# Kernel optimization log

Measured on AMD Instinct MI355X. Metric: run time of the kernel, lower is better.

Reference implementation:

```python
import jax, jax.numpy as jnp
import numpy as np

N_POINTS = 1_000_000
FDIM = 32
GRID = 128  # gx = gy = gz = ceil(20 / 0.15625) = 128
LO, HI = -10.0, 10.0
INIT_STD = 0.05


def setup_inputs() -> dict:
    key = jax.random.key(0)
    k1, k2 = jax.random.split(key)
    # query points inside the bound
    x = jax.random.uniform(k1, (N_POINTS, 3), jnp.float32, LO, HI)
    # dense voxel feature grid, layout [C, D, H, W] (squeezed batch dim)
    feature = jax.random.normal(k2, (FDIM, GRID, GRID, GRID), jnp.float32) * INIT_STD
    return {"x": x, "feature": feature}


def reference(x, feature):
    # normalize_coordinates: map bound -> [-1, 1] per axis (x, y, z order)
    coords = 2.0 * (x - LO) / (HI - LO) - 1.0  # [N, 3]

    C, D, H, W = feature.shape
    # grid_sample, align_corners=False: pixel = ((c + 1) * size - 1) / 2
    fx = ((coords[:, 0] + 1.0) * W - 1.0) * 0.5
    fy = ((coords[:, 1] + 1.0) * H - 1.0) * 0.5
    fz = ((coords[:, 2] + 1.0) * D - 1.0) * 0.5

    x0f, y0f, z0f = jnp.floor(fx), jnp.floor(fy), jnp.floor(fz)
    wx, wy, wz = fx - x0f, fy - y0f, fz - z0f  # trilinear fractions
    x0 = x0f.astype(jnp.int32)
    y0 = y0f.astype(jnp.int32)
    z0 = z0f.astype(jnp.int32)

    feat_flat = feature.reshape(C, -1)  # [C, D*H*W]
    out = jnp.zeros((C, x.shape[0]), dtype=feature.dtype)
    for dz in (0, 1):
        for dy in (0, 1):
            for dx in (0, 1):
                xi, yi, zi = x0 + dx, y0 + dy, z0 + dz
                w = ((wx if dx else 1.0 - wx)
                     * (wy if dy else 1.0 - wy)
                     * (wz if dz else 1.0 - wz))
                # padding_mode='zeros': out-of-range corners contribute 0
                valid = ((xi >= 0) & (xi < W) & (yi >= 0) & (yi < H)
                         & (zi >= 0) & (zi < D))
                idx = ((jnp.clip(zi, 0, D - 1) * H + jnp.clip(yi, 0, H - 1)) * W
                       + jnp.clip(xi, 0, W - 1))
                vals = feat_flat[:, idx]  # gather -> [C, N]
                out = out + vals * (w * valid).astype(feature.dtype)[None, :]
    # transpose(0, 1) -> [N, fdim]
    return out.T
```

## Files before the change

### kernel.cpp

```cpp
#include <hip/hip_runtime.h>
#include <hip/hip_fp16.h>


constexpr int   GD      = 128;
constexpr long long SPATIAL = (long long)GD * GD * GD;
constexpr int   FD      = 32;
constexpr float PLO     = -10.0f;
constexpr float PHI     = 10.0f;

typedef float nfloat4 __attribute__((ext_vector_type(4)));

__global__ __launch_bounds__(256) void transpose_feat_h(
    const float* __restrict__ f, __half* __restrict__ o) {
    __shared__ float lds[64][FD + 1];
    const int t  = threadIdx.x;
    const long long s0 = (long long)blockIdx.x * 64;
    const int sl = t & 63;
    const int cq = t >> 6;
#pragma unroll
    for (int it = 0; it < 8; ++it) {
        const int c = it * 4 + cq;
        lds[sl][c] =
            __builtin_nontemporal_load(f + (size_t)c * SPATIAL + s0 + sl);
    }
    __syncthreads();
    const int c0 = (t & 15) * 2;
    const int sw = t >> 4;
#pragma unroll
    for (int it = 0; it < 4; ++it) {
        const int s = sw + it * 16;
        __half2 h;
        h.x = __float2half(lds[s][c0]);
        h.y = __float2half(lds[s][c0 + 1]);
        *reinterpret_cast<__half2*>(o + (size_t)(s0 + s) * FD + c0) = h;
    }
}

__global__ __launch_bounds__(256) void trilerp_h(
    const float* __restrict__ x, const __half* __restrict__ ft,
    float* __restrict__ out, int npts) {
    const int tid = blockIdx.x * 256 + threadIdx.x;
    const int n = tid >> 2;
    if (n >= npts) return;
    const int j = tid & 3;

    const float px = x[3 * n + 0];
    const float py = x[3 * n + 1];
    const float pz = x[3 * n + 2];

    const float cx = 2.0f * (px - PLO) / (PHI - PLO) - 1.0f;
    const float cy = 2.0f * (py - PLO) / (PHI - PLO) - 1.0f;
    const float cz = 2.0f * (pz - PLO) / (PHI - PLO) - 1.0f;
    const float fx = ((cx + 1.0f) * GD - 1.0f) * 0.5f;
    const float fy = ((cy + 1.0f) * GD - 1.0f) * 0.5f;
    const float fz = ((cz + 1.0f) * GD - 1.0f) * 0.5f;

    const float x0f = floorf(fx), y0f = floorf(fy), z0f = floorf(fz);
    const float wx = fx - x0f, wy = fy - y0f, wz = fz - z0f;
    const int x0 = (int)x0f, y0 = (int)y0f, z0 = (int)z0f;

    float acc[8] = {0.f, 0.f, 0.f, 0.f, 0.f, 0.f, 0.f, 0.f};
#pragma unroll
    for (int dz = 0; dz < 2; ++dz) {
#pragma unroll
        for (int dy = 0; dy < 2; ++dy) {
#pragma unroll
            for (int dx = 0; dx < 2; ++dx) {
                const int xi = x0 + dx, yi = y0 + dy, zi = z0 + dz;
                const bool valid = ((unsigned)xi < (unsigned)GD) &
                                   ((unsigned)yi < (unsigned)GD) &
                                   ((unsigned)zi < (unsigned)GD);
                float w = (dx ? wx : 1.0f - wx) * (dy ? wy : 1.0f - wy) *
                          (dz ? wz : 1.0f - wz);
                w = valid ? w : 0.0f;
                const int xc = min(max(xi, 0), GD - 1);
                const int yc = min(max(yi, 0), GD - 1);
                const int zc = min(max(zi, 0), GD - 1);
                const size_t idx = (size_t)(zc * GD + yc) * GD + xc;
                const nfloat4 raw = *reinterpret_cast<const nfloat4*>(
                    ft + idx * FD + j * 8);
                const __half2* h2 = reinterpret_cast<const __half2*>(&raw);
#pragma unroll
                for (int k = 0; k < 4; ++k) {
                    const float2 fv = __half22float2(h2[k]);
                    acc[2 * k + 0] = fmaf(fv.x, w, acc[2 * k + 0]);
                    acc[2 * k + 1] = fmaf(fv.y, w, acc[2 * k + 1]);
                }
            }
        }
    }
    float* op = out + (size_t)n * FD + j * 8;
    nfloat4 o0 = {acc[0], acc[1], acc[2], acc[3]};
    nfloat4 o1 = {acc[4], acc[5], acc[6], acc[7]};
    __builtin_nontemporal_store(o0, reinterpret_cast<nfloat4*>(op));
    __builtin_nontemporal_store(o1, reinterpret_cast<nfloat4*>(op) + 1);
}

__global__ __launch_bounds__(256) void trilerp_direct(
    const float* __restrict__ x, const float* __restrict__ f,
    float* __restrict__ out, int npts) {
    const int tid = blockIdx.x * 256 + threadIdx.x;
    const int n = tid >> 3;
    if (n >= npts) return;
    const int j = tid & 7;

    const float px = x[3 * n + 0];
    const float py = x[3 * n + 1];
    const float pz = x[3 * n + 2];
    const float cx = 2.0f * (px - PLO) / (PHI - PLO) - 1.0f;
    const float cy = 2.0f * (py - PLO) / (PHI - PLO) - 1.0f;
    const float cz = 2.0f * (pz - PLO) / (PHI - PLO) - 1.0f;
    const float fx = ((cx + 1.0f) * GD - 1.0f) * 0.5f;
    const float fy = ((cy + 1.0f) * GD - 1.0f) * 0.5f;
    const float fz = ((cz + 1.0f) * GD - 1.0f) * 0.5f;
    const float x0f = floorf(fx), y0f = floorf(fy), z0f = floorf(fz);
    const float wx = fx - x0f, wy = fy - y0f, wz = fz - z0f;
    const int x0 = (int)x0f, y0 = (int)y0f, z0 = (int)z0f;

    float acc[4] = {0.f, 0.f, 0.f, 0.f};
#pragma unroll
    for (int dz = 0; dz < 2; ++dz)
#pragma unroll
        for (int dy = 0; dy < 2; ++dy)
#pragma unroll
            for (int dx = 0; dx < 2; ++dx) {
                const int xi = x0 + dx, yi = y0 + dy, zi = z0 + dz;
                const bool valid = ((unsigned)xi < (unsigned)GD) &
                                   ((unsigned)yi < (unsigned)GD) &
                                   ((unsigned)zi < (unsigned)GD);
                float w = (dx ? wx : 1.0f - wx) * (dy ? wy : 1.0f - wy) *
                          (dz ? wz : 1.0f - wz);
                w = valid ? w : 0.0f;
                const int xc = min(max(xi, 0), GD - 1);
                const int yc = min(max(yi, 0), GD - 1);
                const int zc = min(max(zi, 0), GD - 1);
                const size_t idx = (size_t)(zc * GD + yc) * GD + xc;
#pragma unroll
                for (int k = 0; k < 4; ++k)
                    acc[k] = fmaf(f[(size_t)(j * 4 + k) * SPATIAL + idx], w, acc[k]);
            }
#pragma unroll
    for (int k = 0; k < 4; ++k) out[(size_t)n * FD + j * 4 + k] = acc[k];
}

extern "C" void kernel_launch(void* const* d_in, const int* in_sizes, int n_in,
                              void* d_out, int out_size, void* d_ws, size_t ws_size,
                              hipStream_t stream) {
    const float* x    = (const float*)d_in[0];
    const float* feat = (const float*)d_in[1];
    float*       out  = (float*)d_out;
    const int npts = in_sizes[0] / 3;

    const size_t need = (size_t)SPATIAL * FD * sizeof(__half);

    if (ws_size >= need) {
        __half* fth = (__half*)d_ws;
        transpose_feat_h<<<(int)(SPATIAL / 64), 256, 0, stream>>>(feat, fth);
        const int gblocks = (npts * 4 + 255) / 256;
        trilerp_h<<<gblocks, 256, 0, stream>>>(x, fth, out, npts);
    } else {
        const int gblocks = (npts * 8 + 255) / 256;
        trilerp_direct<<<gblocks, 256, 0, stream>>>(x, feat, out, npts);
    }
}
```

Baseline: 497.7 us.

## Bin query points by z-slab before trilinear gather to improve locality

```diff
diff --git a/kernel.cpp b/kernel.cpp
--- a/kernel.cpp
+++ b/kernel.cpp
@@ -7,8 +7,16 @@
 constexpr int   FD      = 32;
 constexpr float PLO     = -10.0f;
 constexpr float PHI     = 10.0f;
+constexpr int   NBUCKET = 129;
 
 typedef float nfloat4 __attribute__((ext_vector_type(4)));
+
+__device__ __forceinline__ int z_bucket(float pz) {
+    const float cz = 2.0f * (pz - PLO) / (PHI - PLO) - 1.0f;
+    const float fz = ((cz + 1.0f) * GD - 1.0f) * 0.5f;
+    int zb = (int)floorf(fz) + 1;
+    return min(max(zb, 0), NBUCKET - 1);
+}
 
 __global__ __launch_bounds__(256) void transpose_feat_h(
     const float* __restrict__ f, __half* __restrict__ o) {
@@ -36,17 +44,57 @@
     }
 }
 
-__global__ __launch_bounds__(256) void trilerp_h(
-    const float* __restrict__ x, const __half* __restrict__ ft,
-    float* __restrict__ out, int npts) {
-    const int tid = blockIdx.x * 256 + threadIdx.x;
-    const int n = tid >> 2;
+__global__ __launch_bounds__(256) void hist_kernel(
+    const float* __restrict__ x, int* __restrict__ hist, int npts) {
+    __shared__ int h[NBUCKET];
+    const int t = threadIdx.x;
+    if (t < NBUCKET) h[t] = 0;
+    __syncthreads();
+    const int n = blockIdx.x * 256 + t;
+    if (n < npts) {
+        const int zb = z_bucket(x[3 * n + 2]);
+        atomicAdd(&h[zb], 1);
+    }
+    __syncthreads();
+    if (t < NBUCKET && h[t]) atomicAdd(&hist[t], h[t]);
+}
+
+__global__ void scan_hist(const int* __restrict__ hist,
+                          int* __restrict__ cursor) {
+    if (threadIdx.x == 0 && blockIdx.x == 0) {
+        int run = 0;
+        for (int b = 0; b < NBUCKET; ++b) {
+            cursor[b] = run;
+            run += hist[b];
+        }
+    }
+}
+
+__global__ __launch_bounds__(256) void scatter_kernel(
+    const float* __restrict__ x, int* __restrict__ cursor,
+    nfloat4* __restrict__ binned, int npts) {
+    const int n = blockIdx.x * 256 + threadIdx.x;
     if (n >= npts) return;
-    const int j = tid & 3;
-
     const float px = x[3 * n + 0];
     const float py = x[3 * n + 1];
     const float pz = x[3 * n + 2];
+    const int zb = z_bucket(pz);
+    const int pos = atomicAdd(&cursor[zb], 1);
+    nfloat4 rec = {px, py, pz, __int_as_float(n)};
+    binned[pos] = rec;
+}
+
+__global__ __launch_bounds__(256) void trilerp_b(
+    const nfloat4* __restrict__ binned, const __half* __restrict__ ft,
+    float* __restrict__ out, int npts) {
+    const int tid = blockIdx.x * 256 + threadIdx.x;
+    const int i = tid >> 2;
+    if (i >= npts) return;
+    const int j = tid & 3;
+
+    const nfloat4 rec = binned[i];
+    const float px = rec.x, py = rec.y, pz = rec.z;
+    const int n = __float_as_int(rec.w);
 
     const float cx = 2.0f * (px - PLO) / (PHI - PLO) - 1.0f;
     const float cy = 2.0f * (py - PLO) / (PHI - PLO) - 1.0f;
@@ -96,13 +144,13 @@
     __builtin_nontemporal_store(o1, reinterpret_cast<nfloat4*>(op) + 1);
 }
 
-__global__ __launch_bounds__(256) void trilerp_direct(
-    const float* __restrict__ x, const float* __restrict__ f,
+__global__ __launch_bounds__(256) void trilerp_h(
+    const float* __restrict__ x, const __half* __restrict__ ft,
     float* __restrict__ out, int npts) {
     const int tid = blockIdx.x * 256 + threadIdx.x;
-    const int n = tid >> 3;
+    const int n = tid >> 2;
     if (n >= npts) return;
-    const int j = tid & 7;
+    const int j = tid & 3;
 
     const float px = x[3 * n + 0];
     const float py = x[3 * n + 1];
@@ -117,7 +165,7 @@
     const float wx = fx - x0f, wy = fy - y0f, wz = fz - z0f;
     const int x0 = (int)x0f, y0 = (int)y0f, z0 = (int)z0f;
 
-    float acc[4] = {0.f, 0.f, 0.f, 0.f};
+    float acc[8] = {0.f, 0.f, 0.f, 0.f, 0.f, 0.f, 0.f, 0.f};
 #pragma unroll
     for (int dz = 0; dz < 2; ++dz)
 #pragma unroll
@@ -135,6 +183,62 @@
                 const int yc = min(max(yi, 0), GD - 1);
                 const int zc = min(max(zi, 0), GD - 1);
                 const size_t idx = (size_t)(zc * GD + yc) * GD + xc;
+                const nfloat4 raw = *reinterpret_cast<const nfloat4*>(
+                    ft + idx * FD + j * 8);
+                const __half2* h2 = reinterpret_cast<const __half2*>(&raw);
+#pragma unroll
+                for (int k = 0; k < 4; ++k) {
+                    const float2 fv = __half22float2(h2[k]);
+                    acc[2 * k + 0] = fmaf(fv.x, w, acc[2 * k + 0]);
+                    acc[2 * k + 1] = fmaf(fv.y, w, acc[2 * k + 1]);
+                }
+            }
+    float* op = out + (size_t)n * FD + j * 8;
+    nfloat4 o0 = {acc[0], acc[1], acc[2], acc[3]};
+    nfloat4 o1 = {acc[4], acc[5], acc[6], acc[7]};
+    __builtin_nontemporal_store(o0, reinterpret_cast<nfloat4*>(op));
+    __builtin_nontemporal_store(o1, reinterpret_cast<nfloat4*>(op) + 1);
+}
+
+__global__ __launch_bounds__(256) void trilerp_direct(
+    const float* __restrict__ x, const float* __restrict__ f,
+    float* __restrict__ out, int npts) {
+    const int tid = blockIdx.x * 256 + threadIdx.x;
+    const int n = tid >> 3;
+    if (n >= npts) return;
+    const int j = tid & 7;
+
+    const float px = x[3 * n + 0];
+    const float py = x[3 * n + 1];
+    const float pz = x[3 * n + 2];
+    const float cx = 2.0f * (px - PLO) / (PHI - PLO) - 1.0f;
+    const float cy = 2.0f * (py - PLO) / (PHI - PLO) - 1.0f;
+    const float cz = 2.0f * (pz - PLO) / (PHI - PLO) - 1.0f;
+    const float fx = ((cx + 1.0f) * GD - 1.0f) * 0.5f;
+    const float fy = ((cy + 1.0f) * GD - 1.0f) * 0.5f;
+    const float fz = ((cz + 1.0f) * GD - 1.0f) * 0.5f;
+    const float x0f = floorf(fx), y0f = floorf(fy), z0f = floorf(fz);
+    const float wx = fx - x0f, wy = fy - y0f, wz = fz - z0f;
+    const int x0 = (int)x0f, y0 = (int)y0f, z0 = (int)z0f;
+
+    float acc[4] = {0.f, 0.f, 0.f, 0.f};
+#pragma unroll
+    for (int dz = 0; dz < 2; ++dz)
+#pragma unroll
+        for (int dy = 0; dy < 2; ++dy)
+#pragma unroll
+            for (int dx = 0; dx < 2; ++dx) {
+                const int xi = x0 + dx, yi = y0 + dy, zi = z0 + dz;
+                const bool valid = ((unsigned)xi < (unsigned)GD) &
+                                   ((unsigned)yi < (unsigned)GD) &
+                                   ((unsigned)zi < (unsigned)GD);
+                float w = (dx ? wx : 1.0f - wx) * (dy ? wy : 1.0f - wy) *
+                          (dz ? wz : 1.0f - wz);
+                w = valid ? w : 0.0f;
+                const int xc = min(max(xi, 0), GD - 1);
+                const int yc = min(max(yi, 0), GD - 1);
+                const int zc = min(max(zi, 0), GD - 1);
+                const size_t idx = (size_t)(zc * GD + yc) * GD + xc;
 #pragma unroll
                 for (int k = 0; k < 4; ++k)
                     acc[k] = fmaf(f[(size_t)(j * 4 + k) * SPATIAL + idx], w, acc[k]);
@@ -151,15 +255,34 @@
     float*       out  = (float*)d_out;
     const int npts = in_sizes[0] / 3;
 
-    const size_t need = (size_t)SPATIAL * FD * sizeof(__half);
-
-    if (ws_size >= need) {
+    const size_t FTH_BYTES    = (size_t)SPATIAL * FD * sizeof(__half);
+    const size_t BINNED_OFF   = FTH_BYTES;
+    const size_t BINNED_BYTES = (size_t)npts * 16;
+    const size_t META_OFF     = BINNED_OFF + ((BINNED_BYTES + 255) & ~(size_t)255);
+    const size_t META_BYTES   = 2 * NBUCKET * sizeof(int);
+    const size_t need_binned  = META_OFF + META_BYTES;
+
+    const int pblocks = (npts + 255) / 256;
+    const int gblocks = (npts * 4 + 255) / 256;
+
+    if (ws_size >= need_binned) {
+        __half*  fth    = (__half*)d_ws;
+        nfloat4* binned = (nfloat4*)((char*)d_ws + BINNED_OFF);
+        int*     hist   = (int*)((char*)d_ws + META_OFF);
+        int*     cursor = hist + NBUCKET;
+
+        hipMemsetAsync(hist, 0, NBUCKET * sizeof(int), stream);
+        transpose_feat_h<<<(int)(SPATIAL / 64), 256, 0, stream>>>(feat, fth);
+        hist_kernel<<<pblocks, 256, 0, stream>>>(x, hist, npts);
+        scan_hist<<<1, 64, 0, stream>>>(hist, cursor);
+        scatter_kernel<<<pblocks, 256, 0, stream>>>(x, cursor, binned, npts);
+        trilerp_b<<<gblocks, 256, 0, stream>>>(binned, fth, out, npts);
+    } else if (ws_size >= FTH_BYTES) {
         __half* fth = (__half*)d_ws;
         transpose_feat_h<<<(int)(SPATIAL / 64), 256, 0, stream>>>(feat, fth);
-        const int gblocks = (npts * 4 + 255) / 256;
         trilerp_h<<<gblocks, 256, 0, stream>>>(x, fth, out, npts);
     } else {
-        const int gblocks = (npts * 8 + 255) / 256;
-        trilerp_direct<<<gblocks, 256, 0, stream>>>(x, feat, out, npts);
-    }
-}
+        const int dblocks = (npts * 8 + 255) / 256;
+        trilerp_direct<<<dblocks, 256, 0, stream>>>(x, feat, out, npts);
+    }
+}
```

Result: slower. 1.343 ms (+169.8%).
